# Optimization experiments

Hardware: AMD Instinct MI355X
Metric: run time of the kernel (lower is better)

Reference implementation:

```python
import jax, jax.numpy as jnp
import numpy as np

ANCHORS = jnp.array([[0.57273, 0.677385], [1.87446, 2.06253], [3.33843, 5.47434],
                     [7.88282, 3.52778], [9.77052, 9.16828]], dtype=jnp.float32)
IOU_THR = 0.6
SCALE_NOOBJ = 1.0
SCALE_OBJ = 5.0
DS = 32.0          # downsample_rate
EPS = 1e-7


def _iou_wh(w1, h1, w2, h2):
    # GetCenterAlignIouBetween: boxes aligned at centers -> IoU depends on w,h only
    inter = jnp.minimum(w1, w2) * jnp.minimum(h1, h2)
    return inter / (w1 * h1 + w2 * h2 - inter + EPS)


def setup_inputs() -> dict:
    B, W, H, A, C, M = 128, 19, 19, 5, 81, 24
    N = W * H
    key = jax.random.key(0)
    ks = jax.random.split(key, 8)
    ii, jj = jnp.meshgrid(jnp.arange(W), jnp.arange(H), indexing='ij')
    fm_cord = jnp.stack([jj, ii], -1).reshape(N, 2).astype(jnp.float32)  # (x=j, y=i)
    conf = jax.random.uniform(ks[0], (B, W, H, A, 1)) * 0.98 + 0.01      # valid BCE probs
    pred_xy = fm_cord.reshape(1, W, H, 1, 2) + jax.random.uniform(ks[1], (B, W, H, A, 2))
    pred_wh = jax.random.uniform(ks[2], (B, W, H, A, 2)) * 8.0 + 0.2     # fm units, >0
    cls_score = jax.random.normal(ks[3], (B, W, H, A, C))
    # distinct grid cells per image so sequential scatter == vectorized scatter
    cells = jax.vmap(lambda k: jax.random.choice(k, N, (M,), replace=False))(
        jax.random.split(ks[4], B))
    ci = cells // H
    cj = cells % H
    frac = jax.random.uniform(ks[5], (B, M, 2))
    x = (cj.astype(jnp.float32) + frac[..., 0]) * DS   # pixel coords
    y = (ci.astype(jnp.float32) + frac[..., 1]) * DS
    wh = jax.random.uniform(ks[6], (B, M, 2), minval=12.0, maxval=280.0)
    true_object = jnp.stack([x, y, wh[..., 0], wh[..., 1]], -1)          # [B,M,4] pixels
    labels = jax.random.randint(ks[7], (B, M), 0, C - 1)
    true_label = jax.nn.one_hot(labels, C, dtype=jnp.float32)            # [B,M,C]
    return dict(epoch=0, conf=conf, pred_xy=pred_xy, pred_wh=pred_wh,
                cls_score=cls_score, true_label=true_label,
                true_object=true_object, fm_cord=fm_cord)


def _yolo_loss(conf, pred_xy, pred_wh, cls_score, true_label, true_object, fm_cord):
    B, W, H, A, C = cls_score.shape
    N = W * H
    NA = N * A
    S = float(W)  # config.output_size

    # ---- target assignment (vectorized version of the python loops) ----
    obj = true_object / DS                               # fm units, [B,M,4]
    gx, gy, gw, gh = obj[..., 0], obj[..., 1], obj[..., 2], obj[..., 3]
    i = gy.astype(jnp.int32)                             # row index  (int() truncation)
    j = gx.astype(jnp.int32)                             # col index
    cell = i * H + j                                     # flat cell, [B,M]

    a_iou = _iou_wh(ANCHORS[None, None, :, 0], ANCHORS[None, None, :, 1],
                    gw[..., None], gh[..., None])        # [B,M,A]
    best = jnp.argmax(a_iou, axis=-1)                    # [B,M]
    is_best = best[..., None] == jnp.arange(A)[None, None, :]
    over = a_iou > IOU_THR

    bb = jnp.arange(B)[:, None]
    pwh = pred_wh.reshape(B, N, A, 2)[bb, cell]          # [B,M,A,2] gather at gt cells
    pwh_b = jnp.take_along_axis(pwh, best[..., None, None], axis=2)[:, :, 0]  # [B,M,2]
    iou_pg = _iou_wh(pwh_b[..., 0], pwh_b[..., 1], gw, gh)                    # [B,M]

    mask_val = jnp.where(is_best, 1.0, jnp.where(over, -1.0, 0.0))            # [B,M,A]
    sw = 2.0 - (gw / S) * (gh / S)                                            # [B,M]
    sw_val = jnp.where(is_best, sw[..., None], jnp.where(over, -1.0, 0.0))
    pgi_val = jnp.where(~is_best & over, 0.0, iou_pg[..., None])              # [B,M,A]
    bg = jax.nn.one_hot(C - 1, C, dtype=cls_score.dtype)
    ts_val = jnp.where((is_best | over)[..., None], true_label[:, :, None, :], bg)
    bbox_val = jnp.where(is_best[..., None], obj[:, :, None, :], 0.0)         # [B,M,A,4]

    obj_mask = jnp.zeros((B, N, A)).at[bb, cell].set(mask_val)
    scale_w = jnp.zeros((B, N, A)).at[bb, cell].set(sw_val)
    pgi = jnp.zeros((B, N, A)).at[bb, cell].set(pgi_val)
    true_score = jnp.zeros((B, N, A, C)).at[..., -1].set(1.0).at[bb, cell].set(ts_val)
    true_bbox = jnp.zeros((B, N, A, 4)).at[bb, cell].set(bbox_val)

    # ---- masked losses over flattened [B, W*H*A, ...] ----
    conf_f = conf.reshape(B, NA)
    om = obj_mask.reshape(B, NA)
    swf = scale_w.reshape(B, NA)
    pgif = pgi.reshape(B, NA)
    pxy = pred_xy.reshape(B, NA, 2)
    pwh_f = pred_wh.reshape(B, NA, 2)
    tb = true_bbox.reshape(B, NA, 4)
    ts = true_score.reshape(B, NA, C)
    cs = cls_score.reshape(B, NA, C)
    cord = jnp.repeat(fm_cord[:, None, :], A, axis=1).reshape(NA, 2)

    cp = jnp.clip(conf_f, EPS, 1.0 - EPS)
    noobj_loss = SCALE_NOOBJ * jnp.sum((om == 0) * (-jnp.log(1.0 - cp))) / B
    obj_loss = SCALE_OBJ * jnp.sum(
        (om == 1) * (-(pgif * jnp.log(cp) + (1.0 - pgif) * jnp.log(1.0 - cp)))) / B

    gt = (swf > 0).astype(conf_f.dtype)                  # [B,NA]
    w3 = (SCALE_OBJ * gt * swf)[..., None]
    xy_loss = jnp.sum(w3 * ((pxy - cord[None]) - (tb[..., :2] - cord[None])) ** 2) / B
    wh_loss = jnp.sum(w3 * (pwh_f - tb[..., 2:]) ** 2) / B

    # CE with soft targets, per position: [B,NA]
    ce = -jnp.sum(ts * jax.nn.log_softmax(cs, axis=-1), axis=-1)
    # original broadcasts mask [B,1,NA] * ce [B,NA] -> [B,B,NA] then .sum();
    # equivalent factored form: sum_n (sum_b1 mask) * (sum_b2 ce)
    score_loss = SCALE_OBJ * jnp.sum(gt.sum(0) * ce.sum(0)) / B

    total = noobj_loss + obj_loss + xy_loss + wh_loss + score_loss
    return total, noobj_loss, obj_loss, score_loss, xy_loss, wh_loss


def reference(epoch, conf, pred_xy, pred_wh, cls_score, true_label, true_object, fm_cord):
    return _yolo_loss(conf, pred_xy, pred_wh, cls_score,
                      true_label, true_object, fm_cord)
```

## Files before the change

### kernel.cpp

```cpp
#include <hip/hip_runtime.h>

#define Bsz 128
#define Cd 81
#define Md 24
#define Nd 361
#define NAd 1805
#define RPW 16
#define NT 113
#define NBLK_CLS (NT*16)
#define NBLK_ASSIGN 48
#define NBLK_TOT (NBLK_CLS + NBLK_ASSIGN)
#define NOBJ (Bsz*Md)
#define EPSF 1e-7f
#define IOU_THRF 0.6f

#define OFF_CORR  0
#define OFF_GT    1824
#define OFF_ACC   3648
#define MEMSET_FLOATS 3652
#define OFF_PART  4096
#define OFF_NOOBJ 33024

typedef float vf4 __attribute__((ext_vector_type(4)));

#define EXP4(v) { v.x=__expf(v.x); v.y=__expf(v.y); v.z=__expf(v.z); v.w=__expf(v.w); }
#define NTL4(p) __builtin_nontemporal_load(p)

__global__ __launch_bounds__(64) void yolo_sweep(
        const float* __restrict__ conf,
        const float* __restrict__ pred_xy,
        const float* __restrict__ pred_wh,
        const float* __restrict__ cls_score,
        const float* __restrict__ true_label,
        const float* __restrict__ true_object,
        float* __restrict__ ws) {
    __shared__ float ex[1300];
    const int lane = threadIdx.x;
    const int bid = blockIdx.x;

    if (bid < NBLK_CLS) {
        const int r = lane >> 2, h = lane & 3;
        vf4* l4 = (vf4*)ex;
        const int t = bid >> 4, g = bid & 15;
        const int na0 = (t == NT - 1) ? (NAd - RPW) : t * RPW;
        const int vmin = t * RPW;
        const bool validr = (na0 + r) >= vmin;
        const bool validc = (lane < RPW) && ((na0 + lane) >= vmin);

        float accCE = 0.0f, nb = 0.0f;

        size_t s = ((size_t)(g * 8) * NAd + na0) * Cd;
        size_t a0a = s & ~(size_t)3;
        int mcur = (int)(s & 3);
        const vf4* gp = (const vf4*)cls_score + (a0a >> 2);
        vf4 u0 = NTL4(gp + 0 * 64 + lane);
        vf4 u1 = NTL4(gp + 1 * 64 + lane);
        vf4 u2 = NTL4(gp + 2 * 64 + lane);
        vf4 u3 = NTL4(gp + 3 * 64 + lane);
        vf4 u4 = NTL4(gp + 4 * 64 + lane);
        vf4 u5 = NTL4(gp + 261 + lane);
        float cf = validc ? __builtin_nontemporal_load(conf + (size_t)(g * 8) * NAd + na0 + lane)
                          : 0.5f;

        for (int it = 0; it < 8; ++it) {
            EXP4(u0); EXP4(u1); EXP4(u2); EXP4(u3); EXP4(u4); EXP4(u5);
            l4[0 * 64 + lane] = u0;
            l4[1 * 64 + lane] = u1;
            l4[2 * 64 + lane] = u2;
            l4[3 * 64 + lane] = u3;
            l4[4 * 64 + lane] = u4;
            l4[261 + lane] = u5;
            __builtin_amdgcn_wave_barrier();

            vf4 n0 = {}, n1 = {}, n2 = {}, n3 = {}, n4 = {}, n5 = {};
            float cfn = 0.0f; int mnext = 0;
            if (it < 7) {
                int b = g * 8 + it + 1;
                s = ((size_t)b * NAd + na0) * Cd;
                a0a = s & ~(size_t)3;
                mnext = (int)(s & 3);
                gp = (const vf4*)cls_score + (a0a >> 2);
                n0 = NTL4(gp + 0 * 64 + lane);
                n1 = NTL4(gp + 1 * 64 + lane);
                n2 = NTL4(gp + 2 * 64 + lane);
                n3 = NTL4(gp + 3 * 64 + lane);
                n4 = NTL4(gp + 4 * 64 + lane);
                n5 = NTL4(gp + 261 + lane);
                if (validc)
                    cfn = __builtin_nontemporal_load(conf + (size_t)b * NAd + na0 + lane);
            }

            const float* p = ex + mcur + r * Cd;
            float sacc = 0.0f;
            #pragma unroll
            for (int j = 0; j < 21; j++) {
                int c0 = h * 21 + j;
                int cc = c0 < 81 ? c0 : 80;
                sacc += p[cc] * ((c0 < 81) ? 1.0f : 0.0f);
            }
            sacc += __shfl_xor(sacc, 1, 64);
            sacc += __shfl_xor(sacc, 2, 64);
            if (h == 0 && validr)
                accCE += __logf(sacc) - __logf(p[80]);
            if (validc) {
                float cp = fminf(fmaxf(cf, EPSF), 1.0f - EPSF);
                nb += -__logf(1.0f - cp);
            }

            u0 = n0; u1 = n1; u2 = n2; u3 = n3; u4 = n4; u5 = n5;
            cf = cfn; mcur = mnext;
        }

        if (h == 0 && validr)
            ws[OFF_PART + (size_t)(na0 + r) * 16 + g] = accCE;
        #pragma unroll
        for (int off = 32; off > 0; off >>= 1) nb += __shfl_xor(nb, off, 64);
        if (lane == 0) ws[OFF_NOOBJ + bid] = nb;
    } else {
        const float AW[5] = {0.57273f, 1.87446f, 3.33843f, 7.88282f, 9.77052f};
        const float AH[5] = {0.677385f, 2.06253f, 5.47434f, 3.52778f, 9.16828f};
        const int idx = (bid - NBLK_CLS) * 64 + lane;
        float* corr = ws + OFF_CORR;
        float* gt   = ws + OFF_GT;

        const float* tl = true_label + (size_t)idx * Cd;
        float labf = 0.0f;
        #pragma unroll
        for (int c0 = 0; c0 < Cd; c0++) labf += tl[c0] * (float)c0;
        int lab = (int)(labf + 0.5f);

        int b = idx / Md;
        const float4 to = ((const float4*)true_object)[idx];
        const float inv_ds = 1.0f / 32.0f;
        float gx = to.x * inv_ds, gy = to.y * inv_ds;
        float gw = to.z * inv_ds, gh = to.w * inv_ds;
        int ci = (int)gy, cj = (int)gx;
        int cell = ci * 19 + cj;
        float garea = gw * gh;

        float best_iou = -1.0f; int best = 0; bool over[5];
        #pragma unroll
        for (int a = 0; a < 5; a++) {
            float inter = fminf(AW[a], gw) * fminf(AH[a], gh);
            float iou = inter / (AW[a] * AH[a] + garea - inter + EPSF);
            over[a] = iou > IOU_THRF;
            if (iou > best_iou) { best_iou = iou; best = a; }
        }

        int base_bn = (b * Nd + cell) * 5;
        float pwb = pred_wh[(size_t)(base_bn + best) * 2 + 0];
        float phb = pred_wh[(size_t)(base_bn + best) * 2 + 1];
        float inter = fminf(pwb, gw) * fminf(phb, gh);
        float iou_pg = inter / (pwb * phb + garea - inter + EPSF);
        float sw = 2.0f - (gw * (1.0f / 19.0f)) * (gh * (1.0f / 19.0f));

        float a0 = 0.f, a1 = 0.f, a2 = 0.f, a3 = 0.f;
        #pragma unroll
        for (int a = 0; a < 5; a++) {
            bool isb = (a == best);
            if (!(isb || over[a])) continue;
            int pos = base_bn + a;
            int na  = cell * 5 + a;
            float cp = fminf(fmaxf(conf[pos], EPSF), 1.0f - EPSF);
            a0 += __logf(1.0f - cp);
            const float* cs = cls_score + (size_t)pos * Cd;
            atomicAdd(&corr[na], cs[Cd - 1] - cs[lab]);
            if (isb) {
                atomicAdd(&gt[na], 1.0f);
                a1 += -(iou_pg * __logf(cp) + (1.0f - iou_pg) * __logf(1.0f - cp));
                float px = pred_xy[(size_t)pos * 2 + 0], py = pred_xy[(size_t)pos * 2 + 1];
                a2 += sw * ((px - gx) * (px - gx) + (py - gy) * (py - gy));
                float pwa = pred_wh[(size_t)pos * 2 + 0], pha = pred_wh[(size_t)pos * 2 + 1];
                a3 += sw * ((pwa - gw) * (pwa - gw) + (pha - gh) * (pha - gh));
            }
        }
        #pragma unroll
        for (int off = 32; off > 0; off >>= 1) {
            a0 += __shfl_xor(a0, off, 64);
            a1 += __shfl_xor(a1, off, 64);
            a2 += __shfl_xor(a2, off, 64);
            a3 += __shfl_xor(a3, off, 64);
        }
        if (lane == 0) {
            atomicAdd(&ws[OFF_ACC + 0], a0);
            atomicAdd(&ws[OFF_ACC + 1], a1);
            atomicAdd(&ws[OFF_ACC + 2], a2);
            atomicAdd(&ws[OFF_ACC + 3], a3);
        }
    }
}

__global__ __launch_bounds__(1024) void yolo_reduce(
        const float* __restrict__ ws, float* __restrict__ out) {
    __shared__ float red[2][16];
    const int tid = threadIdx.x;
    float nsum = 0.0f;
    for (int i = tid; i < NBLK_CLS; i += 1024) nsum += ws[OFF_NOOBJ + i];
    float ssum = 0.0f;
    const float4* part4 = (const float4*)(ws + OFF_PART);
    for (int na = tid; na < NAd; na += 1024) {
        float4 p0 = part4[na * 4 + 0];
        float4 p1 = part4[na * 4 + 1];
        float4 p2 = part4[na * 4 + 2];
        float4 p3 = part4[na * 4 + 3];
        float ce = p0.x + p0.y + p0.z + p0.w + p1.x + p1.y + p1.z + p1.w
                 + p2.x + p2.y + p2.z + p2.w + p3.x + p3.y + p3.z + p3.w
                 + ws[OFF_CORR + na];
        ssum += ws[OFF_GT + na] * ce;
    }

    float v[2] = {nsum, ssum};
    #pragma unroll
    for (int k = 0; k < 2; k++) {
        float x = v[k];
        #pragma unroll
        for (int off = 32; off > 0; off >>= 1) x += __shfl_xor(x, off, 64);
        if ((tid & 63) == 0) red[k][tid >> 6] = x;
    }
    __syncthreads();
    if (tid == 0) {
        float t0 = 0.f, t1 = 0.f;
        #pragma unroll
        for (int w = 0; w < 16; w++) { t0 += red[0][w]; t1 += red[1][w]; }
        const float invB = 1.0f / (float)Bsz;
        float noobj = 1.0f * (t0 + ws[OFF_ACC + 0]) * invB;
        float obj   = 5.0f * ws[OFF_ACC + 1] * invB;
        float xy    = 5.0f * ws[OFF_ACC + 2] * invB;
        float wh    = 5.0f * ws[OFF_ACC + 3] * invB;
        float score = 5.0f * t1 * invB;
        out[0] = noobj + obj + xy + wh + score;
        out[1] = noobj;
        out[2] = obj;
        out[3] = score;
        out[4] = xy;
        out[5] = wh;
    }
}

extern "C" void kernel_launch(void* const* d_in, const int* in_sizes, int n_in,
                              void* d_out, int out_size, void* d_ws, size_t ws_size,
                              hipStream_t stream) {
    const float* conf    = (const float*)d_in[1];
    const float* pred_xy = (const float*)d_in[2];
    const float* pred_wh = (const float*)d_in[3];
    const float* cls     = (const float*)d_in[4];
    const float* tlabel  = (const float*)d_in[5];
    const float* tobject = (const float*)d_in[6];
    float* ws  = (float*)d_ws;
    float* out = (float*)d_out;

    hipMemsetAsync(ws, 0, MEMSET_FLOATS * sizeof(float), stream);

    yolo_sweep<<<NBLK_TOT, 64, 0, stream>>>(conf, pred_xy, pred_wh, cls,
                                            tlabel, tobject, ws);

    yolo_reduce<<<1, 1024, 0, stream>>>(ws, out);
}
```

Measured before the change: 134.9 us.

## Replace global atomics and memset with per-object records reduced in shared memory

The assignment blocks now write per-object correction values, target indices and per-block partial sums to the workspace instead of doing global atomicAdds. The reduce kernel scatters these into shared-memory arrays with LDS atomics. This removes the hipMemsetAsync launch and the contended global atomics. The non-temporal load hints on the class-score stream are also dropped in favour of plain float4 loads. The cost is extra workspace writes and a longer serial single-block reduce that must read about 30K extra floats.

```diff
diff --git a/kernel.cpp b/kernel.cpp
--- a/kernel.cpp
+++ b/kernel.cpp
@@ -14,17 +14,14 @@
 #define EPSF 1e-7f
 #define IOU_THRF 0.6f
 
-#define OFF_CORR  0
-#define OFF_GT    1824
-#define OFF_ACC   3648
-#define MEMSET_FLOATS 3652
-#define OFF_PART  4096
-#define OFF_NOOBJ 33024
-
-typedef float vf4 __attribute__((ext_vector_type(4)));
+#define OFF_PART  0
+#define OFF_NOOBJ 28880
+#define OFF_RECNA 30688
+#define OFF_RECV  46048
+#define OFF_GTNA  61408
+#define OFF_ACCS  64480
 
 #define EXP4(v) { v.x=__expf(v.x); v.y=__expf(v.y); v.z=__expf(v.z); v.w=__expf(v.w); }
-#define NTL4(p) __builtin_nontemporal_load(p)
 
 __global__ __launch_bounds__(64) void yolo_sweep(
         const float* __restrict__ conf,
@@ -40,7 +37,7 @@
 
     if (bid < NBLK_CLS) {
         const int r = lane >> 2, h = lane & 3;
-        vf4* l4 = (vf4*)ex;
+        float4* l4 = (float4*)ex;
         const int t = bid >> 4, g = bid & 15;
         const int na0 = (t == NT - 1) ? (NAd - RPW) : t * RPW;
         const int vmin = t * RPW;
@@ -52,15 +49,14 @@
         size_t s = ((size_t)(g * 8) * NAd + na0) * Cd;
         size_t a0a = s & ~(size_t)3;
         int mcur = (int)(s & 3);
-        const vf4* gp = (const vf4*)cls_score + (a0a >> 2);
-        vf4 u0 = NTL4(gp + 0 * 64 + lane);
-        vf4 u1 = NTL4(gp + 1 * 64 + lane);
-        vf4 u2 = NTL4(gp + 2 * 64 + lane);
-        vf4 u3 = NTL4(gp + 3 * 64 + lane);
-        vf4 u4 = NTL4(gp + 4 * 64 + lane);
-        vf4 u5 = NTL4(gp + 261 + lane);
-        float cf = validc ? __builtin_nontemporal_load(conf + (size_t)(g * 8) * NAd + na0 + lane)
-                          : 0.5f;
+        const float4* gp = (const float4*)cls_score + (a0a >> 2);
+        float4 u0 = gp[0 * 64 + lane];
+        float4 u1 = gp[1 * 64 + lane];
+        float4 u2 = gp[2 * 64 + lane];
+        float4 u3 = gp[3 * 64 + lane];
+        float4 u4 = gp[4 * 64 + lane];
+        float4 u5 = gp[261 + lane];
+        float cf = validc ? conf[(size_t)(g * 8) * NAd + na0 + lane] : 0.5f;
 
         for (int it = 0; it < 8; ++it) {
             EXP4(u0); EXP4(u1); EXP4(u2); EXP4(u3); EXP4(u4); EXP4(u5);
@@ -72,22 +68,22 @@
             l4[261 + lane] = u5;
             __builtin_amdgcn_wave_barrier();
 
-            vf4 n0 = {}, n1 = {}, n2 = {}, n3 = {}, n4 = {}, n5 = {};
+            float4 n0 = {}, n1 = {}, n2 = {}, n3 = {}, n4 = {}, n5 = {};
             float cfn = 0.0f; int mnext = 0;
             if (it < 7) {
                 int b = g * 8 + it + 1;
                 s = ((size_t)b * NAd + na0) * Cd;
                 a0a = s & ~(size_t)3;
                 mnext = (int)(s & 3);
-                gp = (const vf4*)cls_score + (a0a >> 2);
-                n0 = NTL4(gp + 0 * 64 + lane);
-                n1 = NTL4(gp + 1 * 64 + lane);
-                n2 = NTL4(gp + 2 * 64 + lane);
-                n3 = NTL4(gp + 3 * 64 + lane);
-                n4 = NTL4(gp + 4 * 64 + lane);
-                n5 = NTL4(gp + 261 + lane);
+                gp = (const float4*)cls_score + (a0a >> 2);
+                n0 = gp[0 * 64 + lane];
+                n1 = gp[1 * 64 + lane];
+                n2 = gp[2 * 64 + lane];
+                n3 = gp[3 * 64 + lane];
+                n4 = gp[4 * 64 + lane];
+                n5 = gp[261 + lane];
                 if (validc)
-                    cfn = __builtin_nontemporal_load(conf + (size_t)b * NAd + na0 + lane);
+                    cfn = conf[(size_t)b * NAd + na0 + lane];
             }
 
             const float* p = ex + mcur + r * Cd;
@@ -119,9 +115,8 @@
     } else {
         const float AW[5] = {0.57273f, 1.87446f, 3.33843f, 7.88282f, 9.77052f};
         const float AH[5] = {0.677385f, 2.06253f, 5.47434f, 3.52778f, 9.16828f};
-        const int idx = (bid - NBLK_CLS) * 64 + lane;
-        float* corr = ws + OFF_CORR;
-        float* gt   = ws + OFF_GT;
+        const int abid = bid - NBLK_CLS;
+        const int idx = abid * 64 + lane;
 
         const float* tl = true_label + (size_t)idx * Cd;
         float labf = 0.0f;
@@ -158,22 +153,28 @@
         #pragma unroll
         for (int a = 0; a < 5; a++) {
             bool isb = (a == best);
-            if (!(isb || over[a])) continue;
+            bool act = isb || over[a];
             int pos = base_bn + a;
             int na  = cell * 5 + a;
-            float cp = fminf(fmaxf(conf[pos], EPSF), 1.0f - EPSF);
-            a0 += __logf(1.0f - cp);
-            const float* cs = cls_score + (size_t)pos * Cd;
-            atomicAdd(&corr[na], cs[Cd - 1] - cs[lab]);
-            if (isb) {
-                atomicAdd(&gt[na], 1.0f);
-                a1 += -(iou_pg * __logf(cp) + (1.0f - iou_pg) * __logf(1.0f - cp));
-                float px = pred_xy[(size_t)pos * 2 + 0], py = pred_xy[(size_t)pos * 2 + 1];
-                a2 += sw * ((px - gx) * (px - gx) + (py - gy) * (py - gy));
-                float pwa = pred_wh[(size_t)pos * 2 + 0], pha = pred_wh[(size_t)pos * 2 + 1];
-                a3 += sw * ((pwa - gw) * (pwa - gw) + (pha - gh) * (pha - gh));
-            }
-        }
+            float cv = 0.0f;
+            if (act) {
+                const float* cs = cls_score + (size_t)pos * Cd;
+                cv = cs[Cd - 1] - cs[lab];
+                float cp = fminf(fmaxf(conf[pos], EPSF), 1.0f - EPSF);
+                a0 += __logf(1.0f - cp);
+                if (isb) {
+                    a1 += -(iou_pg * __logf(cp) + (1.0f - iou_pg) * __logf(1.0f - cp));
+                    float px = pred_xy[(size_t)pos * 2 + 0], py = pred_xy[(size_t)pos * 2 + 1];
+                    a2 += sw * ((px - gx) * (px - gx) + (py - gy) * (py - gy));
+                    float pwa = pred_wh[(size_t)pos * 2 + 0], pha = pred_wh[(size_t)pos * 2 + 1];
+                    a3 += sw * ((pwa - gw) * (pwa - gw) + (pha - gh) * (pha - gh));
+                }
+            }
+            ws[OFF_RECNA + (size_t)idx * 5 + a] = act ? (float)na : 0.0f;
+            ws[OFF_RECV  + (size_t)idx * 5 + a] = cv;
+        }
+        ws[OFF_GTNA + idx] = (float)(cell * 5 + best);
+
         #pragma unroll
         for (int off = 32; off > 0; off >>= 1) {
             a0 += __shfl_xor(a0, off, 64);
@@ -182,18 +183,33 @@
             a3 += __shfl_xor(a3, off, 64);
         }
         if (lane == 0) {
-            atomicAdd(&ws[OFF_ACC + 0], a0);
-            atomicAdd(&ws[OFF_ACC + 1], a1);
-            atomicAdd(&ws[OFF_ACC + 2], a2);
-            atomicAdd(&ws[OFF_ACC + 3], a3);
+            ws[OFF_ACCS + abid * 4 + 0] = a0;
+            ws[OFF_ACCS + abid * 4 + 1] = a1;
+            ws[OFF_ACCS + abid * 4 + 2] = a2;
+            ws[OFF_ACCS + abid * 4 + 3] = a3;
         }
     }
 }
 
 __global__ __launch_bounds__(1024) void yolo_reduce(
         const float* __restrict__ ws, float* __restrict__ out) {
-    __shared__ float red[2][16];
+    __shared__ float corr[NAd];
+    __shared__ float gt[NAd];
+    __shared__ float red[6][16];
     const int tid = threadIdx.x;
+
+    for (int i = tid; i < NAd; i += 1024) { corr[i] = 0.0f; gt[i] = 0.0f; }
+    __syncthreads();
+
+    for (int k = tid; k < NOBJ * 5; k += 1024) {
+        float v = ws[OFF_RECV + k];
+        int na = (int)(ws[OFF_RECNA + k] + 0.5f);
+        atomicAdd(&corr[na], v);
+    }
+    for (int i = tid; i < NOBJ; i += 1024)
+        atomicAdd(&gt[(int)(ws[OFF_GTNA + i] + 0.5f)], 1.0f);
+    __syncthreads();
+
     float nsum = 0.0f;
     for (int i = tid; i < NBLK_CLS; i += 1024) nsum += ws[OFF_NOOBJ + i];
     float ssum = 0.0f;
@@ -205,13 +221,20 @@
         float4 p3 = part4[na * 4 + 3];
         float ce = p0.x + p0.y + p0.z + p0.w + p1.x + p1.y + p1.z + p1.w
                  + p2.x + p2.y + p2.z + p2.w + p3.x + p3.y + p3.z + p3.w
-                 + ws[OFF_CORR + na];
-        ssum += ws[OFF_GT + na] * ce;
-    }
-
-    float v[2] = {nsum, ssum};
+                 + corr[na];
+        ssum += gt[na] * ce;
+    }
+    float acc[4] = {0.f, 0.f, 0.f, 0.f};
+    if (tid < NBLK_ASSIGN) {
+        acc[0] = ws[OFF_ACCS + tid * 4 + 0];
+        acc[1] = ws[OFF_ACCS + tid * 4 + 1];
+        acc[2] = ws[OFF_ACCS + tid * 4 + 2];
+        acc[3] = ws[OFF_ACCS + tid * 4 + 3];
+    }
+
+    float v[6] = {nsum, ssum, acc[0], acc[1], acc[2], acc[3]};
     #pragma unroll
-    for (int k = 0; k < 2; k++) {
+    for (int k = 0; k < 6; k++) {
         float x = v[k];
         #pragma unroll
         for (int off = 32; off > 0; off >>= 1) x += __shfl_xor(x, off, 64);
@@ -219,15 +242,20 @@
     }
     __syncthreads();
     if (tid == 0) {
-        float t0 = 0.f, t1 = 0.f;
-        #pragma unroll
-        for (int w = 0; w < 16; w++) { t0 += red[0][w]; t1 += red[1][w]; }
+        float t[6];
+        #pragma unroll
+        for (int k = 0; k < 6; k++) {
+            float x = 0.f;
+            #pragma unroll
+            for (int w = 0; w < 16; w++) x += red[k][w];
+            t[k] = x;
+        }
         const float invB = 1.0f / (float)Bsz;
-        float noobj = 1.0f * (t0 + ws[OFF_ACC + 0]) * invB;
-        float obj   = 5.0f * ws[OFF_ACC + 1] * invB;
-        float xy    = 5.0f * ws[OFF_ACC + 2] * invB;
-        float wh    = 5.0f * ws[OFF_ACC + 3] * invB;
-        float score = 5.0f * t1 * invB;
+        float noobj = 1.0f * (t[0] + t[2]) * invB;
+        float obj   = 5.0f * t[3] * invB;
+        float xy    = 5.0f * t[4] * invB;
+        float wh    = 5.0f * t[5] * invB;
+        float score = 5.0f * t[1] * invB;
         out[0] = noobj + obj + xy + wh + score;
         out[1] = noobj;
         out[2] = obj;
@@ -249,8 +277,6 @@
     float* ws  = (float*)d_ws;
     float* out = (float*)d_out;
 
-    hipMemsetAsync(ws, 0, MEMSET_FLOATS * sizeof(float), stream);
-
     yolo_sweep<<<NBLK_TOT, 64, 0, stream>>>(conf, pred_xy, pred_wh, cls,
                                             tlabel, tobject, ws);
 
```

New measurement: 150.1 us. +11.3%, slower.
